# Optimization experiments

Hardware: AMD Instinct MI355X
Metric: run time of the kernel (lower is better)

Reference implementation:

```python
import jax, jax.numpy as jnp
import numpy as np

D_MODEL = 1024
NUM_HEADS = 16
DEPTH = D_MODEL // NUM_HEADS


def setup_inputs() -> dict:
    key = jax.random.key(0)
    ks = jax.random.split(key, 12)
    B, S = 4, 2048
    scale = 1.0 / np.sqrt(D_MODEL)
    inp = {
        "query": jax.random.normal(ks[0], (B, S, D_MODEL), dtype=jnp.float32),
        "key": jax.random.normal(ks[1], (B, S, D_MODEL), dtype=jnp.float32),
        "value": jax.random.normal(ks[2], (B, S, D_MODEL), dtype=jnp.float32),
        "mask": jnp.zeros((B, 1, 1, S), dtype=jnp.float32),  # 1.0 = masked position
        "Wq": jax.random.normal(ks[3], (D_MODEL, D_MODEL), dtype=jnp.float32) * scale,
        "bq": jnp.zeros((D_MODEL,), dtype=jnp.float32),
        "Wk": jax.random.normal(ks[4], (D_MODEL, D_MODEL), dtype=jnp.float32) * scale,
        "bk": jnp.zeros((D_MODEL,), dtype=jnp.float32),
        "Wv": jax.random.normal(ks[5], (D_MODEL, D_MODEL), dtype=jnp.float32) * scale,
        "bv": jnp.zeros((D_MODEL,), dtype=jnp.float32),
        "Wo": jax.random.normal(ks[6], (D_MODEL, D_MODEL), dtype=jnp.float32) * scale,
        "bo": jnp.zeros((D_MODEL,), dtype=jnp.float32),
    }
    return inp


def _split_heads(x):
    # [B, S, D] -> [B, H, S, depth]
    B, S, _ = x.shape
    return x.reshape(B, S, NUM_HEADS, DEPTH).transpose(0, 2, 1, 3)


def reference(query, key, value, mask, Wq, bq, Wk, bk, Wv, bv, Wo, bo):
    B, Sq, _ = query.shape
    q = _split_heads(query @ Wq + bq)   # [B, H, Sq, d]
    k = _split_heads(key @ Wk + bk)     # [B, H, Sk, d]
    v = _split_heads(value @ Wv + bv)   # [B, H, Sk, d]
    logits = jnp.einsum('bhqd,bhkd->bhqk', q, k) / jnp.sqrt(jnp.float32(DEPTH))
    logits = logits + mask * (-1e9)
    attn = jax.nn.softmax(logits, axis=-1)
    ctx = jnp.einsum('bhqk,bhkd->bhqd', attn, v)        # [B, H, Sq, d]
    ctx = ctx.transpose(0, 2, 1, 3).reshape(B, Sq, D_MODEL)
    return ctx @ Wo + bo
```

## Files before the change

kernel.cpp:

```cpp
#include <hip/hip_runtime.h>
#include <math.h>

#define BB 4
#define SS 2048
#define DDM 1024
#define HH 16
#define MM (BB * SS)

typedef _Float16 f16;
typedef f16 half8 __attribute__((ext_vector_type(8)));
typedef f16 f16x4 __attribute__((ext_vector_type(4)));
typedef float f32x4 __attribute__((ext_vector_type(4)));

#define GLOAD16(g, l)                                                  \
  __builtin_amdgcn_global_load_lds(                                    \
      (const __attribute__((address_space(1))) void*)(g),              \
      (__attribute__((address_space(3))) void*)(l), 16, 0, 0)

__global__ void cvt_f16_k(const float* __restrict__ in, f16* __restrict__ out,
                          int n4) {
  int i = blockIdx.x * blockDim.x + threadIdx.x;
  const int stride = gridDim.x * blockDim.x;
  for (; i < n4; i += stride) {
    const float4 v = reinterpret_cast<const float4*>(in)[i];
    f16x4 o;
    o.x = (f16)v.x; o.y = (f16)v.y; o.z = (f16)v.z; o.w = (f16)v.w;
    reinterpret_cast<f16x4*>(out)[i] = o;
  }
}

__global__ void wtr_k(const float* __restrict__ W, f16* __restrict__ Wt) {
  __shared__ float t[32][33];
  const int bx = blockIdx.x * 32, by = blockIdx.y * 32;
  const int tx = threadIdx.x, ty = threadIdx.y;
#pragma unroll
  for (int i = 0; i < 4; ++i)
    t[ty + i * 8][tx] = W[(size_t)(by + ty + i * 8) * DDM + bx + tx];
  __syncthreads();
#pragma unroll
  for (int i = 0; i < 4; ++i)
    Wt[(size_t)(bx + ty + i * 8) * DDM + by + tx] = (f16)t[tx][ty + i * 8];
}

__global__ __launch_bounds__(256, 2) void gemm_f16_k(
    const f16* __restrict__ A, const f16* __restrict__ Bt,
    const float* __restrict__ bias, void* __restrict__ out, int mode) {
  __shared__ f16 Al[128 * 64];
  __shared__ f16 Bl[128 * 64];
  const int tid = threadIdx.x;
  const int l = tid & 63, w = tid >> 6;
  const int lr = l & 15, lg = l >> 4;
  const int wr = w >> 1, wc = w & 1;
  const int bm = blockIdx.x << 7, bn = blockIdx.y << 7;

  f32x4 acc[4][4];
#pragma unroll
  for (int m = 0; m < 4; ++m)
#pragma unroll
    for (int n = 0; n < 4; ++n) acc[m][n] = (f32x4){0.f, 0.f, 0.f, 0.f};

  const int srow = tid >> 3;
  const int scol = (tid & 7) ^ (srow & 7);
  const f16* Ap = A + (size_t)(bm + srow) * DDM + scol * 8;
  const f16* Bp = Bt + (size_t)(bn + srow) * DDM + scol * 8;

  for (int kk = 0; kk < DDM; kk += 64) {
#pragma unroll
    for (int it = 0; it < 4; ++it) {
      GLOAD16(Ap + (size_t)(it * 32) * DDM + kk, Al + (it * 256 + w * 64) * 8);
      GLOAD16(Bp + (size_t)(it * 32) * DDM + kk, Bl + (it * 256 + w * 64) * 8);
    }
    __syncthreads();
    half8 af[2][4], bf[2][4];
#pragma unroll
    for (int kh = 0; kh < 2; ++kh) {
#pragma unroll
      for (int m = 0; m < 4; ++m) {
        const int row = wr * 64 + m * 16 + lr;
        af[kh][m] = *reinterpret_cast<const half8*>(
            Al + row * 64 + (((kh * 4 + lg) ^ (lr & 7)) * 8));
      }
#pragma unroll
      for (int n = 0; n < 4; ++n) {
        const int row = wc * 64 + n * 16 + lr;
        bf[kh][n] = *reinterpret_cast<const half8*>(
            Bl + row * 64 + (((kh * 4 + lg) ^ (lr & 7)) * 8));
      }
    }
#pragma unroll
    for (int kh = 0; kh < 2; ++kh)
#pragma unroll
      for (int m = 0; m < 4; ++m)
#pragma unroll
        for (int n = 0; n < 4; ++n)
          acc[m][n] = __builtin_amdgcn_mfma_f32_16x16x32_f16(
              af[kh][m], bf[kh][n], acc[m][n], 0, 0, 0);
    __syncthreads();
  }

#pragma unroll
  for (int n = 0; n < 4; ++n) {
    const int gn = bn + wc * 64 + n * 16 + lr;
    const float bv = bias[gn];
#pragma unroll
    for (int m = 0; m < 4; ++m) {
#pragma unroll
      for (int r = 0; r < 4; ++r) {
        const int gm = bm + wr * 64 + m * 16 + lg * 4 + r;
        const float v = acc[m][n][r] + bv;
        if (mode == 0) {
          reinterpret_cast<float*>(out)[(size_t)gm * DDM + gn] = v;
        } else {
          const int b = gm >> 11, s = gm & (SS - 1);
          const int h = gn >> 6, d = gn & 63;
          reinterpret_cast<f16*>(
              out)[(((size_t)(b * HH + h) * SS + s) << 6) + d] = (f16)v;
        }
      }
    }
  }
}

__global__ __launch_bounds__(256, 2) void attn_f16_k(
    const f16* __restrict__ Q, const f16* __restrict__ K,
    const f16* __restrict__ V, const float* __restrict__ mask,
    f16* __restrict__ ctx) {
  __shared__ f16 Kl[64 * 64];
  __shared__ f16 Vl[64 * 66];
  __shared__ f16 Pl[4 * 16 * 66];
  __shared__ float Ml[SS];

  const int tid = threadIdx.x;
  const int l = tid & 63, w = tid >> 6;
  const int lr = l & 15, lg = l >> 4;
  const int qt = blockIdx.x;
  const int bh = blockIdx.y;
  const int b = bh >> 4, h = bh & 15;

  for (int i = tid; i < SS; i += 256) Ml[i] = mask[(size_t)b * SS + i] * -1e9f;

  const size_t qrow = (size_t)bh * SS + qt * 64 + w * 16 + lr;
  half8 qf0 = *reinterpret_cast<const half8*>(Q + qrow * 64 + lg * 8);
  half8 qf1 = *reinterpret_cast<const half8*>(Q + qrow * 64 + 32 + lg * 8);

  float m_s[4], l_s[4];
  f32x4 oa[4];
#pragma unroll
  for (int r = 0; r < 4; ++r) { m_s[r] = -1e30f; l_s[r] = 0.f; }
#pragma unroll
  for (int n = 0; n < 4; ++n) oa[n] = (f32x4){0.f, 0.f, 0.f, 0.f};

  const f16* Kg = K + (size_t)bh * SS * 64;
  const f16* Vg = V + (size_t)bh * SS * 64;

  const int srow = tid >> 3;
  const int scol = (tid & 7) ^ (srow & 7);
  f16* KlU0 = Kl + (w * 64) * 8;
  f16* KlU1 = Kl + (256 + w * 64) * 8;
  const int c0 = tid, c1 = 256 + tid;
  const int vkey0 = c0 >> 3, vd00 = (c0 & 7) * 8;
  const int vkey1 = c1 >> 3, vd01 = (c1 & 7) * 8;
  f16* Pw = Pl + w * (16 * 66);

  const int kx = lr & 7;

  for (int kt = 0; kt < 32; ++kt) {
    __syncthreads();
    const f16* Kt = Kg + (size_t)kt * 64 * 64;
    GLOAD16(Kt + srow * 64 + scol * 8, KlU0);
    GLOAD16(Kt + (32 + srow) * 64 + scol * 8, KlU1);
    const f16* Vtg = Vg + (size_t)kt * 64 * 64;
    uint4 v0 = *reinterpret_cast<const uint4*>(Vtg + vkey0 * 64 + vd00);
    uint4 v1 = *reinterpret_cast<const uint4*>(Vtg + vkey1 * 64 + vd01);
    {
      const f16* p0 = reinterpret_cast<const f16*>(&v0);
      const f16* p1 = reinterpret_cast<const f16*>(&v1);
#pragma unroll
      for (int j = 0; j < 8; ++j) Vl[(vd00 + j) * 66 + vkey0] = p0[j];
#pragma unroll
      for (int j = 0; j < 8; ++j) Vl[(vd01 + j) * 66 + vkey1] = p1[j];
    }
    __syncthreads();

    f32x4 sv[4];
#pragma unroll
    for (int n = 0; n < 4; ++n) {
      f32x4 s = (f32x4){0.f, 0.f, 0.f, 0.f};
      const int krow = (n * 16 + lr) * 64;
      half8 kf0 = *reinterpret_cast<const half8*>(
          Kl + krow + ((lg ^ kx) * 8));
      half8 kf1 = *reinterpret_cast<const half8*>(
          Kl + krow + (((4 + lg) ^ kx) * 8));
      s = __builtin_amdgcn_mfma_f32_16x16x32_f16(qf0, kf0, s, 0, 0, 0);
      s = __builtin_amdgcn_mfma_f32_16x16x32_f16(qf1, kf1, s, 0, 0, 0);
      const float mk = Ml[kt * 64 + n * 16 + lr];
#pragma unroll
      for (int r = 0; r < 4; ++r) sv[n][r] = s[r] * 0.125f + mk;
    }

#pragma unroll
    for (int r = 0; r < 4; ++r) {
      float mx = fmaxf(fmaxf(sv[0][r], sv[1][r]), fmaxf(sv[2][r], sv[3][r]));
      mx = fmaxf(mx, __shfl_xor(mx, 1));
      mx = fmaxf(mx, __shfl_xor(mx, 2));
      mx = fmaxf(mx, __shfl_xor(mx, 4));
      mx = fmaxf(mx, __shfl_xor(mx, 8));
      const float mn = fmaxf(m_s[r], mx);
      const float corr = __expf(m_s[r] - mn);
      float sum = 0.f;
#pragma unroll
      for (int n = 0; n < 4; ++n) {
        const float p = __expf(sv[n][r] - mn);
        sv[n][r] = p;
        sum += p;
      }
      sum += __shfl_xor(sum, 1);
      sum += __shfl_xor(sum, 2);
      sum += __shfl_xor(sum, 4);
      sum += __shfl_xor(sum, 8);
      l_s[r] = l_s[r] * corr + sum;
      m_s[r] = mn;
#pragma unroll
      for (int n = 0; n < 4; ++n) oa[n][r] *= corr;
    }

#pragma unroll
    for (int n = 0; n < 4; ++n)
#pragma unroll
      for (int r = 0; r < 4; ++r)
        Pw[(lg * 4 + r) * 66 + n * 16 + lr] = (f16)sv[n][r];

    half8 pa0 = *reinterpret_cast<const half8*>(Pw + lr * 66 + lg * 8);
    half8 pa1 = *reinterpret_cast<const half8*>(Pw + lr * 66 + 32 + lg * 8);
#pragma unroll
    for (int n = 0; n < 4; ++n) {
      half8 vf0 = *reinterpret_cast<const half8*>(
          Vl + (n * 16 + lr) * 66 + lg * 8);
      half8 vf1 = *reinterpret_cast<const half8*>(
          Vl + (n * 16 + lr) * 66 + 32 + lg * 8);
      oa[n] = __builtin_amdgcn_mfma_f32_16x16x32_f16(pa0, vf0, oa[n], 0, 0, 0);
      oa[n] = __builtin_amdgcn_mfma_f32_16x16x32_f16(pa1, vf1, oa[n], 0, 0, 0);
    }
  }

#pragma unroll
  for (int r = 0; r < 4; ++r) {
    const float inv = 1.0f / l_s[r];
    const int s_g = qt * 64 + w * 16 + lg * 4 + r;
#pragma unroll
    for (int n = 0; n < 4; ++n)
      ctx[((size_t)b * SS + s_g) * DDM + h * 64 + n * 16 + lr] =
          (f16)(oa[n][r] * inv);
  }
}

extern "C" void kernel_launch(void* const* d_in, const int* in_sizes, int n_in,
                              void* d_out, int out_size, void* d_ws,
                              size_t ws_size, hipStream_t stream) {
  const float* query = (const float*)d_in[0];
  const float* key   = (const float*)d_in[1];
  const float* value = (const float*)d_in[2];
  const float* mask  = (const float*)d_in[3];
  const float* Wq = (const float*)d_in[4];
  const float* bq = (const float*)d_in[5];
  const float* Wk = (const float*)d_in[6];
  const float* bk = (const float*)d_in[7];
  const float* Wv = (const float*)d_in[8];
  const float* bv = (const float*)d_in[9];
  const float* Wo = (const float*)d_in[10];
  const float* bo = (const float*)d_in[11];
  float* out = (float*)d_out;

  const size_t E = (size_t)MM * DDM;
  f16* ws = (f16*)d_ws;
  f16* Qh = ws;
  f16* Kh = Qh + E;
  f16* Vh = Kh + E;
  f16* Wt0 = Vh + E;
  f16* Wt1 = Wt0 + (size_t)DDM * DDM;
  f16* Wt2 = Wt1 + (size_t)DDM * DDM;
  f16* Wt3 = Wt2 + (size_t)DDM * DDM;
  f16* Qp = Wt3 + (size_t)DDM * DDM;
  f16* Kp = Qp + E;
  f16* Vp = Kp + E;
  f16* Ch = Vp + E;

  const int n4 = (int)(E / 4);
  cvt_f16_k<<<2048, 256, 0, stream>>>(query, Qh, n4);
  cvt_f16_k<<<2048, 256, 0, stream>>>(key, Kh, n4);
  cvt_f16_k<<<2048, 256, 0, stream>>>(value, Vh, n4);
  dim3 tb(32, 8), tg(32, 32);
  wtr_k<<<tg, tb, 0, stream>>>(Wq, Wt0);
  wtr_k<<<tg, tb, 0, stream>>>(Wk, Wt1);
  wtr_k<<<tg, tb, 0, stream>>>(Wv, Wt2);
  wtr_k<<<tg, tb, 0, stream>>>(Wo, Wt3);

  dim3 gg(MM / 128, DDM / 128);
  gemm_f16_k<<<gg, 256, 0, stream>>>(Qh, Wt0, bq, Qp, 1);
  gemm_f16_k<<<gg, 256, 0, stream>>>(Kh, Wt1, bk, Kp, 1);
  gemm_f16_k<<<gg, 256, 0, stream>>>(Vh, Wt2, bv, Vp, 1);
  attn_f16_k<<<dim3(SS / 64, BB * HH), 256, 0, stream>>>(Qp, Kp, Vp, mask, Ch);
  gemm_f16_k<<<gg, 256, 0, stream>>>(Ch, Wt3, bo, out, 0);
}
```

Measured before the change: 574.6 us.

## Double-buffer GEMM and attention tiles, emit V pre-transposed from projection

Double-buffers the shared-memory tiles in both the projection GEMM and the attention kernel, so async global-to-LDS loads of the next tile overlap with MFMA work on the current one. The V projection GEMM gains a mode that writes V as [b,h,d,s] with vectorised f16x4 stores. The attention kernel can then load V tiles with direct global_load_lds and a swizzled layout, replacing the per-element transposing LDS scatter. This doubles LDS use per block, which may reduce occupancy, and the V projection now writes with a strided pattern.

Result: faster. 525.8 us (-8.5%).

```diff
diff --git a/kernel.cpp b/kernel.cpp
--- a/kernel.cpp
+++ b/kernel.cpp
@@ -45,8 +45,8 @@
 __global__ __launch_bounds__(256, 2) void gemm_f16_k(
     const f16* __restrict__ A, const f16* __restrict__ Bt,
     const float* __restrict__ bias, void* __restrict__ out, int mode) {
-  __shared__ f16 Al[128 * 64];
-  __shared__ f16 Bl[128 * 64];
+  __shared__ f16 Al[2][128 * 64];
+  __shared__ f16 Bl[2][128 * 64];
   const int tid = threadIdx.x;
   const int l = tid & 63, w = tid >> 6;
   const int lr = l & 15, lg = l >> 4;
@@ -63,40 +63,49 @@
   const int scol = (tid & 7) ^ (srow & 7);
   const f16* Ap = A + (size_t)(bm + srow) * DDM + scol * 8;
   const f16* Bp = Bt + (size_t)(bn + srow) * DDM + scol * 8;
+  const int kx = lr & 7;
+
+#define G_STAGE(buf, kk)                                                     \
+  do {                                                                       \
+    _Pragma("unroll") for (int it = 0; it < 4; ++it) {                       \
+      GLOAD16(Ap + (size_t)(it * 32) * DDM + (kk),                           \
+              &Al[buf][(it * 256 + w * 64) * 8]);                            \
+      GLOAD16(Bp + (size_t)(it * 32) * DDM + (kk),                           \
+              &Bl[buf][(it * 256 + w * 64) * 8]);                            \
+    }                                                                        \
+  } while (0)
+
+  G_STAGE(0, 0);
+  __syncthreads();
 
   for (int kk = 0; kk < DDM; kk += 64) {
-#pragma unroll
-    for (int it = 0; it < 4; ++it) {
-      GLOAD16(Ap + (size_t)(it * 32) * DDM + kk, Al + (it * 256 + w * 64) * 8);
-      GLOAD16(Bp + (size_t)(it * 32) * DDM + kk, Bl + (it * 256 + w * 64) * 8);
-    }
-    __syncthreads();
-    half8 af[2][4], bf[2][4];
+    const int cur = (kk >> 6) & 1;
+    if (kk + 64 < DDM) G_STAGE(cur ^ 1, kk + 64);
 #pragma unroll
     for (int kh = 0; kh < 2; ++kh) {
+      half8 af[4], bf[4];
 #pragma unroll
       for (int m = 0; m < 4; ++m) {
         const int row = wr * 64 + m * 16 + lr;
-        af[kh][m] = *reinterpret_cast<const half8*>(
-            Al + row * 64 + (((kh * 4 + lg) ^ (lr & 7)) * 8));
+        af[m] = *reinterpret_cast<const half8*>(
+            &Al[cur][row * 64 + (((kh * 4 + lg) ^ kx) * 8)]);
       }
 #pragma unroll
       for (int n = 0; n < 4; ++n) {
         const int row = wc * 64 + n * 16 + lr;
-        bf[kh][n] = *reinterpret_cast<const half8*>(
-            Bl + row * 64 + (((kh * 4 + lg) ^ (lr & 7)) * 8));
+        bf[n] = *reinterpret_cast<const half8*>(
+            &Bl[cur][row * 64 + (((kh * 4 + lg) ^ kx) * 8)]);
       }
-    }
-#pragma unroll
-    for (int kh = 0; kh < 2; ++kh)
 #pragma unroll
       for (int m = 0; m < 4; ++m)
 #pragma unroll
         for (int n = 0; n < 4; ++n)
-          acc[m][n] = __builtin_amdgcn_mfma_f32_16x16x32_f16(
-              af[kh][m], bf[kh][n], acc[m][n], 0, 0, 0);
+          acc[m][n] = __builtin_amdgcn_mfma_f32_16x16x32_f16(af[m], bf[n],
+                                                             acc[m][n], 0, 0, 0);
+    }
     __syncthreads();
   }
+#undef G_STAGE
 
 #pragma unroll
   for (int n = 0; n < 4; ++n) {
@@ -104,17 +113,29 @@
     const float bv = bias[gn];
 #pragma unroll
     for (int m = 0; m < 4; ++m) {
-#pragma unroll
-      for (int r = 0; r < 4; ++r) {
-        const int gm = bm + wr * 64 + m * 16 + lg * 4 + r;
-        const float v = acc[m][n][r] + bv;
-        if (mode == 0) {
-          reinterpret_cast<float*>(out)[(size_t)gm * DDM + gn] = v;
-        } else {
-          const int b = gm >> 11, s = gm & (SS - 1);
-          const int h = gn >> 6, d = gn & 63;
-          reinterpret_cast<f16*>(
-              out)[(((size_t)(b * HH + h) * SS + s) << 6) + d] = (f16)v;
+      const int gm0 = bm + wr * 64 + m * 16 + lg * 4;
+      if (mode == 2) {
+        const int b = gm0 >> 11, s = gm0 & (SS - 1);
+        const int h = gn >> 6, d = gn & 63;
+        f16x4 o;
+#pragma unroll
+        for (int r = 0; r < 4; ++r) o[r] = (f16)(acc[m][n][r] + bv);
+        *reinterpret_cast<f16x4*>(
+            reinterpret_cast<f16*>(out) +
+            (((size_t)(b * HH + h) * 64 + d) * SS + s)) = o;
+      } else {
+#pragma unroll
+        for (int r = 0; r < 4; ++r) {
+          const int gm = gm0 + r;
+          const float v = acc[m][n][r] + bv;
+          if (mode == 0) {
+            reinterpret_cast<float*>(out)[(size_t)gm * DDM + gn] = v;
+          } else {
+            const int b = gm >> 11, s = gm & (SS - 1);
+            const int h = gn >> 6, d = gn & 63;
+            reinterpret_cast<f16*>(
+                out)[(((size_t)(b * HH + h) * SS + s) << 6) + d] = (f16)v;
+          }
         }
       }
     }
@@ -123,10 +144,10 @@
 
 __global__ __launch_bounds__(256, 2) void attn_f16_k(
     const f16* __restrict__ Q, const f16* __restrict__ K,
-    const f16* __restrict__ V, const float* __restrict__ mask,
+    const f16* __restrict__ Vt, const float* __restrict__ mask,
     f16* __restrict__ ctx) {
-  __shared__ f16 Kl[64 * 64];
-  __shared__ f16 Vl[64 * 66];
+  __shared__ f16 Kl[2][64 * 64];
+  __shared__ f16 Vl[2][64 * 64];
   __shared__ f16 Pl[4 * 16 * 66];
   __shared__ float Ml[SS];
 
@@ -151,36 +172,30 @@
   for (int n = 0; n < 4; ++n) oa[n] = (f32x4){0.f, 0.f, 0.f, 0.f};
 
   const f16* Kg = K + (size_t)bh * SS * 64;
-  const f16* Vg = V + (size_t)bh * SS * 64;
+  const f16* Vg = Vt + (size_t)bh * 64 * SS;
 
   const int srow = tid >> 3;
   const int scol = (tid & 7) ^ (srow & 7);
-  f16* KlU0 = Kl + (w * 64) * 8;
-  f16* KlU1 = Kl + (256 + w * 64) * 8;
-  const int c0 = tid, c1 = 256 + tid;
-  const int vkey0 = c0 >> 3, vd00 = (c0 & 7) * 8;
-  const int vkey1 = c1 >> 3, vd01 = (c1 & 7) * 8;
+  const int kx = lr & 7;
   f16* Pw = Pl + w * (16 * 66);
 
-  const int kx = lr & 7;
+#define A_STAGE(buf, kt)                                                     \
+  do {                                                                       \
+    const f16* Kt_ = Kg + (size_t)(kt) * 64 * 64;                            \
+    GLOAD16(Kt_ + srow * 64 + scol * 8, &Kl[buf][(w * 64) * 8]);             \
+    GLOAD16(Kt_ + (32 + srow) * 64 + scol * 8,                               \
+            &Kl[buf][(256 + w * 64) * 8]);                                   \
+    const f16* Vr_ = Vg + (size_t)(kt) * 64 + scol * 8;                      \
+    GLOAD16(Vr_ + (size_t)srow * SS, &Vl[buf][(w * 64) * 8]);                \
+    GLOAD16(Vr_ + (size_t)(32 + srow) * SS, &Vl[buf][(256 + w * 64) * 8]);   \
+  } while (0)
+
+  A_STAGE(0, 0);
+  __syncthreads();
 
   for (int kt = 0; kt < 32; ++kt) {
-    __syncthreads();
-    const f16* Kt = Kg + (size_t)kt * 64 * 64;
-    GLOAD16(Kt + srow * 64 + scol * 8, KlU0);
-    GLOAD16(Kt + (32 + srow) * 64 + scol * 8, KlU1);
-    const f16* Vtg = Vg + (size_t)kt * 64 * 64;
-    uint4 v0 = *reinterpret_cast<const uint4*>(Vtg + vkey0 * 64 + vd00);
-    uint4 v1 = *reinterpret_cast<const uint4*>(Vtg + vkey1 * 64 + vd01);
-    {
-      const f16* p0 = reinterpret_cast<const f16*>(&v0);
-      const f16* p1 = reinterpret_cast<const f16*>(&v1);
-#pragma unroll
-      for (int j = 0; j < 8; ++j) Vl[(vd00 + j) * 66 + vkey0] = p0[j];
-#pragma unroll
-      for (int j = 0; j < 8; ++j) Vl[(vd01 + j) * 66 + vkey1] = p1[j];
-    }
-    __syncthreads();
+    const int cur = kt & 1;
+    if (kt + 1 < 32) A_STAGE(cur ^ 1, kt + 1);
 
     f32x4 sv[4];
 #pragma unroll
@@ -188,9 +203,9 @@
       f32x4 s = (f32x4){0.f, 0.f, 0.f, 0.f};
       const int krow = (n * 16 + lr) * 64;
       half8 kf0 = *reinterpret_cast<const half8*>(
-          Kl + krow + ((lg ^ kx) * 8));
+          &Kl[cur][krow + ((lg ^ kx) * 8)]);
       half8 kf1 = *reinterpret_cast<const half8*>(
-          Kl + krow + (((4 + lg) ^ kx) * 8));
+          &Kl[cur][krow + (((4 + lg) ^ kx) * 8)]);
       s = __builtin_amdgcn_mfma_f32_16x16x32_f16(qf0, kf0, s, 0, 0, 0);
       s = __builtin_amdgcn_mfma_f32_16x16x32_f16(qf1, kf1, s, 0, 0, 0);
       const float mk = Ml[kt * 64 + n * 16 + lr];
@@ -234,14 +249,17 @@
     half8 pa1 = *reinterpret_cast<const half8*>(Pw + lr * 66 + 32 + lg * 8);
 #pragma unroll
     for (int n = 0; n < 4; ++n) {
+      const int vrow = (n * 16 + lr) * 64;
       half8 vf0 = *reinterpret_cast<const half8*>(
-          Vl + (n * 16 + lr) * 66 + lg * 8);
+          &Vl[cur][vrow + ((lg ^ kx) * 8)]);
       half8 vf1 = *reinterpret_cast<const half8*>(
-          Vl + (n * 16 + lr) * 66 + 32 + lg * 8);
+          &Vl[cur][vrow + (((4 + lg) ^ kx) * 8)]);
       oa[n] = __builtin_amdgcn_mfma_f32_16x16x32_f16(pa0, vf0, oa[n], 0, 0, 0);
       oa[n] = __builtin_amdgcn_mfma_f32_16x16x32_f16(pa1, vf1, oa[n], 0, 0, 0);
     }
-  }
+    __syncthreads();
+  }
+#undef A_STAGE
 
 #pragma unroll
   for (int r = 0; r < 4; ++r) {
@@ -298,7 +316,7 @@
   dim3 gg(MM / 128, DDM / 128);
   gemm_f16_k<<<gg, 256, 0, stream>>>(Qh, Wt0, bq, Qp, 1);
   gemm_f16_k<<<gg, 256, 0, stream>>>(Kh, Wt1, bk, Kp, 1);
-  gemm_f16_k<<<gg, 256, 0, stream>>>(Vh, Wt2, bv, Vp, 1);
+  gemm_f16_k<<<gg, 256, 0, stream>>>(Vh, Wt2, bv, Vp, 2);
   attn_f16_k<<<dim3(SS / 64, BB * HH), 256, 0, stream>>>(Qp, Kp, Vp, mask, Ch);
   gemm_f16_k<<<gg, 256, 0, stream>>>(Ch, Wt3, bo, out, 0);
 }
```
